# Performance work log

Hardware: AMD Instinct MI355X
Metric: run time of the kernel (lower is better)

## Reference

```python
import jax, jax.numpy as jnp
import numpy as np

B, S, E, H = 2, 2048, 1024, 16
D = E // H  # head_dim = 64


def setup_inputs() -> dict:
    key = jax.random.key(0)
    ks = jax.random.split(key, 8)
    lim = float(np.sqrt(6.0 / (E + E)))  # xavier_uniform
    inp = {
        "query": jax.random.normal(ks[0], (B, S, E), jnp.float32),
        "key": jax.random.normal(ks[1], (B, S, E), jnp.float32),
        "value": jax.random.normal(ks[2], (B, S, E), jnp.float32),
        "Wq": jax.random.uniform(ks[3], (E, E), jnp.float32, -lim, lim),
        "Wk": jax.random.uniform(ks[4], (E, E), jnp.float32, -lim, lim),
        "Wv": jax.random.uniform(ks[5], (E, E), jnp.float32, -lim, lim),
        "Wo": jax.random.uniform(ks[6], (E, E), jnp.float32, -lim, lim),
        "bq": jnp.zeros((E,), jnp.float32),
        "bk": jnp.zeros((E,), jnp.float32),
        "bv": jnp.zeros((E,), jnp.float32),
        "bo": jnp.zeros((E,), jnp.float32),
        # causal mask: True = masked (strictly upper triangular)
        "attn_mask": jnp.triu(jnp.ones((S, S), jnp.bool_), k=1),
    }
    return inp


def reference(query, key, value, Wq, Wk, Wv, Wo, bq, bk, bv, bo, attn_mask):
    # W stored as (in, out); torch Linear equivalent y = x @ W + b
    scaling = D ** (-0.5)
    q = (query @ Wq + bq) * scaling            # (B,S,E), first scaling (MHA.forward)
    k = key @ Wk + bk
    v = value @ Wv + bv
    # split heads -> (B, H, S, D)
    q = q.reshape(B, S, H, D).transpose(0, 2, 1, 3)
    k = k.reshape(B, S, H, D).transpose(0, 2, 1, 3)
    v = v.reshape(B, S, H, D).transpose(0, 2, 1, 3)
    # second scaling inside ScaledDotProductAttention (faithful double-scale)
    scores = jnp.einsum("bhqd,bhkd->bhqk", q, k) / jnp.sqrt(jnp.float32(D))
    scores = jnp.where(attn_mask[None, None, :, :], -jnp.inf, scores)
    attn = jax.nn.softmax(scores, axis=-1)     # dropout is identity in eval
    out = jnp.einsum("bhqk,bhkd->bhqd", attn, v)
    out = out.transpose(0, 2, 1, 3).reshape(B, S, E)
    return out @ Wo + bo
```

## Files before the change

### kernel.cpp

```cpp
#include <hip/hip_runtime.h>
#include <stdint.h>

#define B_ 2
#define S_ 2048
#define E_ 1024
#define H_ 16
#define D_ 64

typedef __attribute__((ext_vector_type(8))) short bf16x8;
typedef __attribute__((ext_vector_type(4))) float f32x4;
typedef __attribute__((ext_vector_type(4))) short s16x4_t;

__device__ __forceinline__ short bfbits(float x) {
    union { float f; uint32_t u; } v; v.f = x;
    uint32_t r = v.u + 0x7fffu + ((v.u >> 16) & 1u);
    return (short)(r >> 16);
}
__device__ __forceinline__ short bfbits_trunc(float x) {
    union { float f; uint32_t u; } v; v.f = x;
    return (short)(v.u >> 16);
}

__device__ __forceinline__ void async16(const short* g, short* l) {
    __builtin_amdgcn_global_load_lds((const __attribute__((address_space(1))) void*)g,
                                     (__attribute__((address_space(3))) void*)l,
                                     16, 0, 0);
}

__global__ __launch_bounds__(256) void cvt_all(const float* __restrict__ q,
                                               const float* __restrict__ k,
                                               const float* __restrict__ v,
                                               const float* __restrict__ Wq,
                                               const float* __restrict__ Wk,
                                               const float* __restrict__ Wv,
                                               const float* __restrict__ Wo,
                                               short* __restrict__ dstX,
                                               short* __restrict__ dstW) {
    __shared__ short t[64][72];
    int bid = blockIdx.x;
    if (bid < 12288) {
        const long long NV = 1048576;
        long long i = (long long)bid * 256 + threadIdx.x;
        const float* src = (i < NV) ? q : (i < 2 * NV) ? k : v;
        long long j = (i >= 2 * NV) ? (i - 2 * NV) : (i >= NV) ? (i - NV) : i;
        float4 x = ((const float4*)src)[j];
        s16x4_t o;
        o[0] = bfbits(x.x); o[1] = bfbits(x.y); o[2] = bfbits(x.z); o[3] = bfbits(x.w);
        ((s16x4_t*)dstX)[i] = o;
        return;
    }
    int wbid = bid - 12288;
    int z = wbid >> 8;
    const float* W = (z == 0) ? Wq : (z == 1) ? Wk : (z == 2) ? Wv : Wo;
    short* o = dstW + (size_t)z * 1048576;
    int rem = wbid & 255;
    int n0 = (rem & 15) * 64, k0 = (rem >> 4) * 64;
    int tid = threadIdx.x;
    int r = tid >> 4, c4 = tid & 15;
    for (int rep = 0; rep < 4; rep++) {
        int kk = rep * 16 + r;
        float4 x = *(const float4*)&W[(size_t)(k0 + kk) * 1024 + n0 + c4 * 4];
        t[c4 * 4 + 0][kk] = bfbits(x.x);
        t[c4 * 4 + 1][kk] = bfbits(x.y);
        t[c4 * 4 + 2][kk] = bfbits(x.z);
        t[c4 * 4 + 3][kk] = bfbits(x.w);
    }
    __syncthreads();
    int n = tid >> 3, c8 = tid & 7;
    for (int rep = 0; rep < 2; rep++) {
        int nn = rep * 32 + n;
        bf16x8 vv;
        for (int jj = 0; jj < 8; jj++) vv[jj] = t[nn][c8 * 8 + jj];
        *(bf16x8*)&o[(size_t)(n0 + nn) * 1024 + k0 + c8 * 8] = vv;
    }
}

__device__ __forceinline__ void gemm_core(const short* __restrict__ A,
                                          const short* __restrict__ Bt,
                                          const float* __restrict__ bias,
                                          short* __restrict__ outB,
                                          float* __restrict__ outF,
                                          int mode, float scale,
                                          int m0, int n0) {
    __shared__ short As[2][128 * 32];
    __shared__ short Bs[2][128 * 32];
    int tid = threadIdx.x, lane = tid & 63, w = tid >> 6;
    int col = lane & 15, quad = lane >> 4;
    int wm = (w >> 1) * 64, wn = (w & 1) * 64;
    f32x4 acc[4][4];
    for (int i = 0; i < 4; i++)
        for (int j = 0; j < 4; j++) acc[i][j] = (f32x4){0.f, 0.f, 0.f, 0.f};

    int r4 = lane >> 2;
    int skoff = ((lane & 3) ^ ((r4 >> 1) & 3)) * 8;
    const short* ga = A + (size_t)(m0 + r4) * 1024 + skoff;
    const short* gb = Bt + (size_t)(n0 + r4) * 1024 + skoff;
    int fro = (quad ^ ((col >> 1) & 3)) * 8;

    auto stage = [&](int t, int b) {
        int k0_ = t * 32;
        for (int c = 0; c < 2; ++c) {
            int rb = w * 32 + c * 16;
            async16(ga + (size_t)rb * 1024 + k0_, &As[b][rb * 32]);
            async16(gb + (size_t)rb * 1024 + k0_, &Bs[b][rb * 32]);
        }
    };

    stage(0, 0);
    __syncthreads();
    for (int t = 0; t < 32; ++t) {
        int cur = t & 1;
        if (t + 1 < 32) stage(t + 1, cur ^ 1);
        bf16x8 af[4], bfr[4];
        for (int i = 0; i < 4; i++)
            af[i] = *(const bf16x8*)&As[cur][(wm + i * 16 + col) * 32 + fro];
        for (int j = 0; j < 4; j++)
            bfr[j] = *(const bf16x8*)&Bs[cur][(wn + j * 16 + col) * 32 + fro];
        for (int i = 0; i < 4; i++)
            for (int j = 0; j < 4; j++)
                acc[i][j] = __builtin_amdgcn_mfma_f32_16x16x32_bf16(af[i], bfr[j], acc[i][j], 0, 0, 0);
        __syncthreads();
    }

    int mbase = m0 + wm + quad * 4;
    for (int i = 0; i < 4; i++) {
        int mb = mbase + i * 16;
        for (int j = 0; j < 4; j++) {
            int n = n0 + wn + j * 16 + col;
            float bv_ = bias[n];
            if (mode == 0) {
                for (int r = 0; r < 4; r++)
                    outB[(size_t)(mb + r) * 1024 + n] = bfbits((acc[i][j][r] + bv_) * scale);
            } else if (mode == 1) {
                int b_ = mb >> 11, s_ = mb & 2047;
                size_t base = (((size_t)(b_ * 16 + (n >> 6)) * 64) + (n & 63)) * 2048 + s_;
                s16x4_t pv;
                for (int r = 0; r < 4; r++) pv[r] = bfbits((acc[i][j][r] + bv_) * scale);
                *(s16x4_t*)&outB[base] = pv;
            } else {
                for (int r = 0; r < 4; r++)
                    outF[(size_t)(mb + r) * 1024 + n] = (acc[i][j][r] + bv_) * scale;
            }
        }
    }
}

#define QSCALE (0.015625f * 1.44269504088896340736f)
__global__ __launch_bounds__(256) void gemm_qkv(const short* __restrict__ Xb,
                                                const short* __restrict__ Wb,
                                                const float* __restrict__ bq,
                                                const float* __restrict__ bk,
                                                const float* __restrict__ bv,
                                                short* __restrict__ Qp) {
    int bid = blockIdx.x;
    int L = (bid & 7) * 96 + (bid >> 3);
    int z = L >> 8;
    int rem = L & 255;
    int m0 = (rem >> 3) * 128, n0 = (rem & 7) * 128;
    const short* A = Xb + (size_t)z * 4194304;
    const short* Bt = Wb + (size_t)z * 1048576;
    const float* bias = (z == 0) ? bq : (z == 1) ? bk : bv;
    short* outB = Qp + (size_t)z * 4194304;
    gemm_core(A, Bt, bias, outB, nullptr, (z == 2) ? 1 : 0, (z == 0) ? QSCALE : 1.0f,
              m0, n0);
}

__global__ __launch_bounds__(256) void gemm_o(const short* __restrict__ Ctx,
                                              const short* __restrict__ Wob,
                                              const float* __restrict__ bo,
                                              float* __restrict__ out) {
    int bid = blockIdx.x;
    int L = (bid & 7) * 32 + (bid >> 3);
    int m0 = (L >> 3) * 128, n0 = (L & 7) * 128;
    gemm_core(Ctx, Wob, bo, nullptr, out, 2, 1.0f, m0, n0);
}

__device__ __forceinline__ void stage_kv(const short* __restrict__ Kp,
                                         const short* __restrict__ VpT,
                                         short* Kbuf, short* Vbuf,
                                         int b, int bh, int h, int kv0,
                                         int lane, int w) {
    int r8 = lane >> 3;
    int sk = ((lane & 7) ^ r8) * 8;
    for (int c = 0; c < 2; c++) {
        int rb = (c * 4 + w) * 8;
        async16(Kp + (size_t)(b * 2048 + kv0 + rb + r8) * 1024 + h * 64 + sk,
                &Kbuf[rb * 64]);
        async16(VpT + (size_t)(bh * 64 + rb + r8) * 2048 + kv0 + sk,
                &Vbuf[rb * 64]);
    }
}

__global__ __launch_bounds__(256) void attn_kernel(const short* __restrict__ Qp,
                                                   const short* __restrict__ Kp,
                                                   const short* __restrict__ VpT,
                                                   short* __restrict__ Ctx) {
    __shared__ short Kt[2][64 * 64];
    __shared__ short Vt[2][64 * 64];
    __shared__ short Pl[8][16 * 72];
    int tid = threadIdx.x, lane = tid & 63, w = tid >> 6;
    int col = lane & 15, quad = lane >> 4;
    int c7 = col & 7;
    int bid = blockIdx.x;
    int L = (bid & 7) * 64 + (bid >> 3);
    int qx = L & 15, bh = L >> 4;
    int b = bh >> 4, h = bh & 15;
    int qtA = qx, qtB = 31 - qx;
    int nA = qtA + 1, nB = qtB + 1;
    int qrowA = qtA * 64 + w * 16, qrowB = qtB * 64 + w * 16;

    bf16x8 ones;
    for (int j = 0; j < 8; j++) ones[j] = (short)0x3F80;

    bf16x8 aqA0, aqA1, aqB0, aqB1;
    {
        const short* qa = Qp + ((size_t)(b * 2048 + qrowA + col)) * 1024 + h * 64;
        aqA0 = *(const bf16x8*)(qa + quad * 8);
        aqA1 = *(const bf16x8*)(qa + 32 + quad * 8);
        const short* qb = Qp + ((size_t)(b * 2048 + qrowB + col)) * 1024 + h * 64;
        aqB0 = *(const bf16x8*)(qb + quad * 8);
        aqB1 = *(const bf16x8*)(qb + 32 + quad * 8);
    }
    f32x4 oA[4], oB[4];
    for (int dj = 0; dj < 4; dj++) {
        oA[dj] = (f32x4){0.f, 0.f, 0.f, 0.f};
        oB[dj] = (f32x4){0.f, 0.f, 0.f, 0.f};
    }
    f32x4 psvA = (f32x4){0.f, 0.f, 0.f, 0.f};
    f32x4 psvB = (f32x4){0.f, 0.f, 0.f, 0.f};

    short* PlA = Pl[w * 2];
    short* PlB = Pl[w * 2 + 1];

    stage_kv(Kp, VpT, Kt[0], Vt[0], b, bh, h, 0, lane, w);

    int t = 0;
    for (; t < nA; ++t) {
        __syncthreads();
        stage_kv(Kp, VpT, Kt[(t + 1) & 1], Vt[(t + 1) & 1], b, bh, h,
                 (t + 1) * 64, lane, w);
        const short* Kb = Kt[t & 1];
        const short* Vb = Vt[t & 1];

        f32x4 sfA[4], sfB[4];
        for (int i = 0; i < 4; i++) {
            sfA[i] = (f32x4){0.f, 0.f, 0.f, 0.f};
            sfB[i] = (f32x4){0.f, 0.f, 0.f, 0.f};
        }
        __builtin_amdgcn_s_setprio(1);
        for (int ks = 0; ks < 2; ks++) {
            bf16x8 bqA = ks ? aqA1 : aqA0;
            bf16x8 bqB = ks ? aqB1 : aqB0;
            int sl = ((ks * 4 + quad) ^ c7) * 8;
            for (int i = 0; i < 4; i++) {
                bf16x8 ak_ = *(const bf16x8*)&Kb[(i * 16 + col) * 64 + sl];
                sfB[i] = __builtin_amdgcn_mfma_f32_16x16x32_bf16(ak_, bqB, sfB[i], 0, 0, 0);
                sfA[i] = __builtin_amdgcn_mfma_f32_16x16x32_bf16(ak_, bqA, sfA[i], 0, 0, 0);
            }
        }
        __builtin_amdgcn_s_setprio(0);
        if (t == nA - 1) {
            int qg = qrowA + col;
            for (int i = 0; i < 4; i++) {
                int kvg = t * 64 + i * 16 + quad * 4;
                for (int r = 0; r < 4; r++)
                    if (kvg + r > qg) sfA[i][r] = -3.0e38f;
            }
        }
        for (int i = 0; i < 4; i++) {
            s16x4_t pw;
            for (int r = 0; r < 4; r++) pw[r] = bfbits_trunc(exp2f(sfB[i][r]));
            *(s16x4_t*)&PlB[col * 72 + i * 16 + quad * 4] = pw;
        }
        for (int i = 0; i < 4; i++) {
            s16x4_t pw;
            for (int r = 0; r < 4; r++) pw[r] = bfbits_trunc(exp2f(sfA[i][r]));
            *(s16x4_t*)&PlA[col * 72 + i * 16 + quad * 4] = pw;
        }
        __builtin_amdgcn_s_setprio(1);
        for (int ks = 0; ks < 2; ks++) {
            bf16x8 apB = *(const bf16x8*)&PlB[col * 72 + ks * 32 + quad * 8];
            bf16x8 apA = *(const bf16x8*)&PlA[col * 72 + ks * 32 + quad * 8];
            int sl = ((ks * 4 + quad) ^ c7) * 8;
            psvB = __builtin_amdgcn_mfma_f32_16x16x32_bf16(apB, ones, psvB, 0, 0, 0);
            psvA = __builtin_amdgcn_mfma_f32_16x16x32_bf16(apA, ones, psvA, 0, 0, 0);
            for (int dj = 0; dj < 4; dj++) {
                bf16x8 bv_ = *(const bf16x8*)&Vb[(dj * 16 + col) * 64 + sl];
                oB[dj] = __builtin_amdgcn_mfma_f32_16x16x32_bf16(apB, bv_, oB[dj], 0, 0, 0);
                oA[dj] = __builtin_amdgcn_mfma_f32_16x16x32_bf16(apA, bv_, oA[dj], 0, 0, 0);
            }
        }
        __builtin_amdgcn_s_setprio(0);
    }
    for (; t < nB; ++t) {
        __syncthreads();
        if (t + 1 < nB)
            stage_kv(Kp, VpT, Kt[(t + 1) & 1], Vt[(t + 1) & 1], b, bh, h,
                     (t + 1) * 64, lane, w);
        const short* Kb = Kt[t & 1];
        const short* Vb = Vt[t & 1];

        f32x4 sfB[4];
        for (int i = 0; i < 4; i++) sfB[i] = (f32x4){0.f, 0.f, 0.f, 0.f};
        __builtin_amdgcn_s_setprio(1);
        for (int ks = 0; ks < 2; ks++) {
            bf16x8 bqB = ks ? aqB1 : aqB0;
            int sl = ((ks * 4 + quad) ^ c7) * 8;
            for (int i = 0; i < 4; i++) {
                bf16x8 ak_ = *(const bf16x8*)&Kb[(i * 16 + col) * 64 + sl];
                sfB[i] = __builtin_amdgcn_mfma_f32_16x16x32_bf16(ak_, bqB, sfB[i], 0, 0, 0);
            }
        }
        __builtin_amdgcn_s_setprio(0);
        if (t == nB - 1) {
            int qg = qrowB + col;
            for (int i = 0; i < 4; i++) {
                int kvg = t * 64 + i * 16 + quad * 4;
                for (int r = 0; r < 4; r++)
                    if (kvg + r > qg) sfB[i][r] = -3.0e38f;
            }
        }
        for (int i = 0; i < 4; i++) {
            s16x4_t pw;
            for (int r = 0; r < 4; r++) pw[r] = bfbits_trunc(exp2f(sfB[i][r]));
            *(s16x4_t*)&PlB[col * 72 + i * 16 + quad * 4] = pw;
        }
        __builtin_amdgcn_s_setprio(1);
        for (int ks = 0; ks < 2; ks++) {
            bf16x8 apB = *(const bf16x8*)&PlB[col * 72 + ks * 32 + quad * 8];
            int sl = ((ks * 4 + quad) ^ c7) * 8;
            psvB = __builtin_amdgcn_mfma_f32_16x16x32_bf16(apB, ones, psvB, 0, 0, 0);
            for (int dj = 0; dj < 4; dj++) {
                bf16x8 bv_ = *(const bf16x8*)&Vb[(dj * 16 + col) * 64 + sl];
                oB[dj] = __builtin_amdgcn_mfma_f32_16x16x32_bf16(apB, bv_, oB[dj], 0, 0, 0);
            }
        }
        __builtin_amdgcn_s_setprio(0);
    }

    float invA[4], invB[4];
    for (int r = 0; r < 4; r++) {
        invA[r] = 1.0f / psvA[r];
        invB[r] = 1.0f / psvB[r];
    }
    for (int r = 0; r < 4; r++) {
        for (int dj = 0; dj < 4; dj++) {
            Ctx[((size_t)(b * 2048 + qrowA + quad * 4 + r)) * 1024 + h * 64 + dj * 16 + col] =
                bfbits(oA[dj][r] * invA[r]);
            Ctx[((size_t)(b * 2048 + qrowB + quad * 4 + r)) * 1024 + h * 64 + dj * 16 + col] =
                bfbits(oB[dj][r] * invB[r]);
        }
    }
}

extern "C" void kernel_launch(void* const* d_in, const int* in_sizes, int n_in,
                              void* d_out, int out_size, void* d_ws, size_t ws_size,
                              hipStream_t stream) {
    const float* q  = (const float*)d_in[0];
    const float* k  = (const float*)d_in[1];
    const float* v  = (const float*)d_in[2];
    const float* Wq = (const float*)d_in[3];
    const float* Wk = (const float*)d_in[4];
    const float* Wv = (const float*)d_in[5];
    const float* Wo = (const float*)d_in[6];
    const float* bq = (const float*)d_in[7];
    const float* bk = (const float*)d_in[8];
    const float* bv = (const float*)d_in[9];
    const float* bo = (const float*)d_in[10];

    short* wsb = (short*)d_ws;
    short* Wb  = wsb;
    short* Xb  = Wb + 4 * 1048576;
    short* Qp  = Xb + 3 * 4194304;
    short* Kp  = Qp + 4194304;
    short* VpT = Kp + 4194304;
    short* Ctx = VpT + 4194304;

    cvt_all<<<13312, 256, 0, stream>>>(q, k, v, Wq, Wk, Wv, Wo, Xb, Wb);
    gemm_qkv<<<768, 256, 0, stream>>>(Xb, Wb, bq, bk, bv, Qp);
    attn_kernel<<<512, 256, 0, stream>>>(Qp, Kp, VpT, Ctx);
    gemm_o<<<256, 256, 0, stream>>>(Ctx, Wb + 3 * 1048576, bo, (float*)d_out);
}
```

Before: 240.3 us.

## Load K/V MFMA operands directly from global memory instead of LDS staging

New measurement: 311.0 us. +29.4%, slower.

```diff
diff --git a/kernel.cpp b/kernel.cpp
--- a/kernel.cpp
+++ b/kernel.cpp
@@ -175,32 +175,13 @@
     gemm_core(Ctx, Wob, bo, nullptr, out, 2, 1.0f, m0, n0);
 }
 
-__device__ __forceinline__ void stage_kv(const short* __restrict__ Kp,
-                                         const short* __restrict__ VpT,
-                                         short* Kbuf, short* Vbuf,
-                                         int b, int bh, int h, int kv0,
-                                         int lane, int w) {
-    int r8 = lane >> 3;
-    int sk = ((lane & 7) ^ r8) * 8;
-    for (int c = 0; c < 2; c++) {
-        int rb = (c * 4 + w) * 8;
-        async16(Kp + (size_t)(b * 2048 + kv0 + rb + r8) * 1024 + h * 64 + sk,
-                &Kbuf[rb * 64]);
-        async16(VpT + (size_t)(bh * 64 + rb + r8) * 2048 + kv0 + sk,
-                &Vbuf[rb * 64]);
-    }
-}
-
 __global__ __launch_bounds__(256) void attn_kernel(const short* __restrict__ Qp,
                                                    const short* __restrict__ Kp,
                                                    const short* __restrict__ VpT,
                                                    short* __restrict__ Ctx) {
-    __shared__ short Kt[2][64 * 64];
-    __shared__ short Vt[2][64 * 64];
     __shared__ short Pl[8][16 * 72];
     int tid = threadIdx.x, lane = tid & 63, w = tid >> 6;
     int col = lane & 15, quad = lane >> 4;
-    int c7 = col & 7;
     int bid = blockIdx.x;
     int L = (bid & 7) * 64 + (bid >> 3);
     int qx = L & 15, bh = L >> 4;
@@ -221,6 +202,13 @@
         aqB0 = *(const bf16x8*)(qb + quad * 8);
         aqB1 = *(const bf16x8*)(qb + 32 + quad * 8);
     }
+    const short* kbase[4];
+    for (int i = 0; i < 4; i++)
+        kbase[i] = Kp + ((size_t)(b * 2048 + i * 16 + col)) * 1024 + h * 64 + quad * 8;
+    const short* vbase[4];
+    for (int dj = 0; dj < 4; dj++)
+        vbase[dj] = VpT + ((size_t)(bh * 64 + dj * 16 + col)) * 2048 + quad * 8;
+
     f32x4 oA[4], oB[4];
     for (int dj = 0; dj < 4; dj++) {
         oA[dj] = (f32x4){0.f, 0.f, 0.f, 0.f};
@@ -232,15 +220,10 @@
     short* PlA = Pl[w * 2];
     short* PlB = Pl[w * 2 + 1];
 
-    stage_kv(Kp, VpT, Kt[0], Vt[0], b, bh, h, 0, lane, w);
-
     int t = 0;
     for (; t < nA; ++t) {
-        __syncthreads();
-        stage_kv(Kp, VpT, Kt[(t + 1) & 1], Vt[(t + 1) & 1], b, bh, h,
-                 (t + 1) * 64, lane, w);
-        const short* Kb = Kt[t & 1];
-        const short* Vb = Vt[t & 1];
+        size_t kt = (size_t)t << 16;
+        size_t vt = (size_t)t * 64;
 
         f32x4 sfA[4], sfB[4];
         for (int i = 0; i < 4; i++) {
@@ -251,9 +234,8 @@
         for (int ks = 0; ks < 2; ks++) {
             bf16x8 bqA = ks ? aqA1 : aqA0;
             bf16x8 bqB = ks ? aqB1 : aqB0;
-            int sl = ((ks * 4 + quad) ^ c7) * 8;
             for (int i = 0; i < 4; i++) {
-                bf16x8 ak_ = *(const bf16x8*)&Kb[(i * 16 + col) * 64 + sl];
+                bf16x8 ak_ = *(const bf16x8*)(kbase[i] + kt + ks * 32);
                 sfB[i] = __builtin_amdgcn_mfma_f32_16x16x32_bf16(ak_, bqB, sfB[i], 0, 0, 0);
                 sfA[i] = __builtin_amdgcn_mfma_f32_16x16x32_bf16(ak_, bqA, sfA[i], 0, 0, 0);
             }
@@ -281,11 +263,10 @@
         for (int ks = 0; ks < 2; ks++) {
             bf16x8 apB = *(const bf16x8*)&PlB[col * 72 + ks * 32 + quad * 8];
             bf16x8 apA = *(const bf16x8*)&PlA[col * 72 + ks * 32 + quad * 8];
-            int sl = ((ks * 4 + quad) ^ c7) * 8;
             psvB = __builtin_amdgcn_mfma_f32_16x16x32_bf16(apB, ones, psvB, 0, 0, 0);
             psvA = __builtin_amdgcn_mfma_f32_16x16x32_bf16(apA, ones, psvA, 0, 0, 0);
             for (int dj = 0; dj < 4; dj++) {
-                bf16x8 bv_ = *(const bf16x8*)&Vb[(dj * 16 + col) * 64 + sl];
+                bf16x8 bv_ = *(const bf16x8*)(vbase[dj] + vt + ks * 32);
                 oB[dj] = __builtin_amdgcn_mfma_f32_16x16x32_bf16(apB, bv_, oB[dj], 0, 0, 0);
                 oA[dj] = __builtin_amdgcn_mfma_f32_16x16x32_bf16(apA, bv_, oA[dj], 0, 0, 0);
             }
@@ -293,21 +274,16 @@
         __builtin_amdgcn_s_setprio(0);
     }
     for (; t < nB; ++t) {
-        __syncthreads();
-        if (t + 1 < nB)
-            stage_kv(Kp, VpT, Kt[(t + 1) & 1], Vt[(t + 1) & 1], b, bh, h,
-                     (t + 1) * 64, lane, w);
-        const short* Kb = Kt[t & 1];
-        const short* Vb = Vt[t & 1];
+        size_t kt = (size_t)t << 16;
+        size_t vt = (size_t)t * 64;
 
         f32x4 sfB[4];
         for (int i = 0; i < 4; i++) sfB[i] = (f32x4){0.f, 0.f, 0.f, 0.f};
         __builtin_amdgcn_s_setprio(1);
         for (int ks = 0; ks < 2; ks++) {
             bf16x8 bqB = ks ? aqB1 : aqB0;
-            int sl = ((ks * 4 + quad) ^ c7) * 8;
             for (int i = 0; i < 4; i++) {
-                bf16x8 ak_ = *(const bf16x8*)&Kb[(i * 16 + col) * 64 + sl];
+                bf16x8 ak_ = *(const bf16x8*)(kbase[i] + kt + ks * 32);
                 sfB[i] = __builtin_amdgcn_mfma_f32_16x16x32_bf16(ak_, bqB, sfB[i], 0, 0, 0);
             }
         }
@@ -328,10 +304,9 @@
         __builtin_amdgcn_s_setprio(1);
         for (int ks = 0; ks < 2; ks++) {
             bf16x8 apB = *(const bf16x8*)&PlB[col * 72 + ks * 32 + quad * 8];
-            int sl = ((ks * 4 + quad) ^ c7) * 8;
             psvB = __builtin_amdgcn_mfma_f32_16x16x32_bf16(apB, ones, psvB, 0, 0, 0);
             for (int dj = 0; dj < 4; dj++) {
-                bf16x8 bv_ = *(const bf16x8*)&Vb[(dj * 16 + col) * 64 + sl];
+                bf16x8 bv_ = *(const bf16x8*)(vbase[dj] + vt + ks * 32);
                 oB[dj] = __builtin_amdgcn_mfma_f32_16x16x32_bf16(apB, bv_, oB[dj], 0, 0, 0);
             }
         }
```
